# Optimization experiments

Hardware: AMD Instinct MI355X
Metric: run time of the kernel (lower is better)

Reference implementation:

```python
import jax, jax.numpy as jnp
import numpy as np

N, L, D = 1024, 64, 1024  # turns, max_len, d_model

def setup_inputs() -> dict:
    key = jax.random.key(0)
    questions = jax.random.normal(key, (N, L, D), dtype=jnp.float32)
    return {"questions": questions}

def reference(questions):
    # avg[i] = mean(questions[:i], axis=0); avg[0] = 0
    # Replace the original O(n^2) Python loop with a single prefix-sum.
    n = questions.shape[0]
    csum = jnp.cumsum(questions, axis=0)                       # [n, L, D]
    denom = jnp.arange(1, n, dtype=questions.dtype)[:, None, None]
    avg = jnp.concatenate(
        [jnp.zeros_like(questions[:1]), csum[:-1] / denom], axis=0
    )                                                          # [n, L, D]
    return jnp.concatenate([questions, avg], axis=-1)          # [n, L, 2D]
```

## Files before the change

### kernel.cpp

```cpp
#include <hip/hip_runtime.h>

constexpr int N_TURNS = 1024;
constexpr int L_LEN   = 64;
constexpr int D_MOD   = 1024;
constexpr unsigned COLS = L_LEN * D_MOD;
constexpr unsigned ROW_STRIDE_OUT = 2u * D_MOD * L_LEN;

__global__ __launch_bounds__(256) void qflow_scan_kernel(
        const float* __restrict__ q, float* __restrict__ out) {
    unsigned c = blockIdx.x * 256u + threadIdx.x;
    unsigned l = c >> 10;
    unsigned d = c & (D_MOD - 1);

    const float* qp = q + c;
    float* op = out + (size_t)l * (2u * D_MOD) + d;
    float run = 0.0f;
    #pragma unroll 32
    for (unsigned i = 0; i < N_TURNS; ++i) {
        float v = qp[(size_t)i * COLS];
        float inv = (i == 0) ? 0.0f : __builtin_amdgcn_rcpf((float)i);
        float avg = run * inv;
        size_t ob = (size_t)i * ROW_STRIDE_OUT;
        op[ob] = v;
        op[ob + D_MOD] = avg;
        run += v;
    }
}

extern "C" void kernel_launch(void* const* d_in, const int* in_sizes, int n_in,
                              void* d_out, int out_size, void* d_ws, size_t ws_size,
                              hipStream_t stream) {
    const float* q = (const float*)d_in[0];
    float* out = (float*)d_out;
    qflow_scan_kernel<<<COLS / 256, 256, 0, stream>>>(q, out);
}
```

Measured before the change: 153.6 us.

## Split scan over turns across four waves with shared-memory chunk prefix

Each block now handles 64 columns, and its four waves each scan a 64-turn chunk. Per-wave chunk sums are combined through shared memory to produce carry-in prefixes, so the serial dependency along turns is shortened and there are four times as many blocks for latency hiding. Each thread holds 64 loaded values in registers so it can make a second pass for the outputs. This risks register pressure and adds two barriers per super-step. Output addressing is rebased with a plus/minus 512 offset.

```diff
diff --git a/kernel.cpp b/kernel.cpp
--- a/kernel.cpp
+++ b/kernel.cpp
@@ -1,29 +1,65 @@
 #include <hip/hip_runtime.h>
 
 constexpr int N_TURNS = 1024;
-constexpr int L_LEN   = 64;
 constexpr int D_MOD   = 1024;
-constexpr unsigned COLS = L_LEN * D_MOD;
-constexpr unsigned ROW_STRIDE_OUT = 2u * D_MOD * L_LEN;
+constexpr unsigned COLS = 65536;
+constexpr unsigned OUT_ROW = 2u * 64 * D_MOD;
 
-__global__ __launch_bounds__(256) void qflow_scan_kernel(
+constexpr int WAVES = 4;
+constexpr int RPW   = 64;
+constexpr int SUPER = N_TURNS / (WAVES * RPW);
+
+__global__ __launch_bounds__(256, 4) void qflow_block_scan(
         const float* __restrict__ q, float* __restrict__ out) {
-    unsigned c = blockIdx.x * 256u + threadIdx.x;
-    unsigned l = c >> 10;
-    unsigned d = c & (D_MOD - 1);
+    __shared__ float csum[WAVES][64];
+
+    const unsigned lane = threadIdx.x & 63u;
+    const unsigned w    = threadIdx.x >> 6;
+    const unsigned c    = blockIdx.x * 64u + lane;
+    const unsigned l    = c >> 10;
+    const unsigned d    = c & (D_MOD - 1u);
 
     const float* qp = q + c;
-    float* op = out + (size_t)l * (2u * D_MOD) + d;
-    float run = 0.0f;
-    #pragma unroll 32
-    for (unsigned i = 0; i < N_TURNS; ++i) {
-        float v = qp[(size_t)i * COLS];
-        float inv = (i == 0) ? 0.0f : __builtin_amdgcn_rcpf((float)i);
-        float avg = run * inv;
-        size_t ob = (size_t)i * ROW_STRIDE_OUT;
-        op[ob] = v;
-        op[ob + D_MOD] = avg;
-        run += v;
+    float* opb = out + (size_t)l * (2u * D_MOD) + d + 512u;
+
+    float superPrefix = 0.0f;
+
+    for (unsigned s = 0; s < SUPER; ++s) {
+        const unsigned base = s * (WAVES * RPW) + w * RPW;
+        float v[RPW];
+
+        #pragma unroll
+        for (int j = 0; j < RPW; ++j) {
+            v[j] = qp[(size_t)(base + j) * COLS];
+        }
+        float chunk = 0.0f;
+        #pragma unroll
+        for (int j = 0; j < RPW; ++j) chunk += v[j];
+
+        csum[w][lane] = chunk;
+        __syncthreads();
+
+        float run = superPrefix;
+        float total = 0.0f;
+        #pragma unroll
+        for (int w2 = 0; w2 < WAVES; ++w2) {
+            float t = csum[w2][lane];
+            if ((unsigned)w2 < w) run += t;
+            total += t;
+        }
+        __syncthreads();
+
+        #pragma unroll
+        for (int j = 0; j < RPW; ++j) {
+            const unsigned i = base + j;
+            const float inv = (i == 0) ? 0.0f : __builtin_amdgcn_rcpf((float)i);
+            const float avg = run * inv;
+            const size_t ob = (size_t)i * OUT_ROW;
+            opb[ob - 512] = v[j];
+            opb[ob + 512] = avg;
+            run += v[j];
+        }
+        superPrefix += total;
     }
 }
 
@@ -32,5 +68,5 @@
                               hipStream_t stream) {
     const float* q = (const float*)d_in[0];
     float* out = (float*)d_out;
-    qflow_scan_kernel<<<COLS / 256, 256, 0, stream>>>(q, out);
+    qflow_block_scan<<<COLS / 64, 256, 0, stream>>>(q, out);
 }
```

After: 178.9 us. +16.5%, slower.
